# Kernel optimization log

Hardware: AMD Instinct MI355X
Metric: run time of the kernel (lower is better)

The kernel has to match this reference:

```python
import jax, jax.numpy as jnp
import numpy as np

B, T, C = 1, 2048, 1024
H = 16
HD = C // H
BLOCK = 2048
NEG = float('-inf')

def setup_inputs() -> dict:
    key = jax.random.key(0)
    ks = jax.random.split(key, 6)
    x = jax.random.normal(ks[0], (B, T, C), dtype=jnp.float32)
    cumulative_scores = jax.random.normal(ks[1], (B, T), dtype=jnp.float32) * 0.1
    padding_mask = jnp.ones((B, T), dtype=jnp.float32)
    token_index = jax.random.randint(ks[2], (B, T), 0, BLOCK).astype(jnp.int64)
    w_attn = jax.random.normal(ks[3], (C, 3 * C), dtype=jnp.float32) * (1.0 / np.sqrt(C))
    b_attn = jnp.zeros((3 * C,), dtype=jnp.float32)
    w_proj = jax.random.normal(ks[4], (C, C), dtype=jnp.float32) * (1.0 / np.sqrt(C))
    b_proj = jnp.zeros((C,), dtype=jnp.float32)
    return dict(x=x, cumulative_scores=cumulative_scores, padding_mask=padding_mask,
                token_index=token_index, w_attn=w_attn, b_attn=b_attn,
                w_proj=w_proj, b_proj=b_proj)

def _rotate_half(z):
    z1, z2 = z[..., : z.shape[-1] // 2], z[..., z.shape[-1] // 2 :]
    return jnp.concatenate((-z2, z1), axis=-1)

def reference(x, cumulative_scores, padding_mask, token_index, w_attn, b_attn, w_proj, b_proj):
    # fused QKV projection
    qkv = x @ w_attn + b_attn                      # (B,T,3C)
    q, k, v = jnp.split(qkv, 3, axis=2)
    q = q.reshape(B, T, H, HD).transpose(0, 2, 1, 3)  # (B,H,T,HD)
    k = k.reshape(B, T, H, HD).transpose(0, 2, 1, 3)
    v = v.reshape(B, T, H, HD).transpose(0, 2, 1, 3)

    # dynamic per-token RoPE positions: global token counts (original scatter
    # broadcasts indices over batch, so counts are global across all batches)
    cnt = jnp.zeros((BLOCK,), jnp.float32).at[token_index.reshape(-1)].add(1.0)
    per_tok = (1.0 / (cnt + 1e-10))[token_index]       # (B,T)
    partial = jnp.cumsum(per_tok, axis=-1)             # (B,T) fractional positions

    inv_freq = 1.0 / (10000.0 ** (jnp.arange(0, HD, 2, dtype=jnp.float32) / HD))
    freqs = partial[..., None] * inv_freq              # (B,T,HD/2)
    emb = jnp.concatenate((freqs, freqs), axis=-1)     # (B,T,HD)
    cos = jnp.cos(emb)[:, None]                        # (B,1,T,HD)
    sin = jnp.sin(emb)[:, None]
    q = q * cos + _rotate_half(q) * sin
    k = k * cos + _rotate_half(k) * sin

    # 'fork' plan: overwrite last channel
    q = q.at[..., -1].set(1.0)
    k = k.at[..., -1].set(jnp.broadcast_to(cumulative_scores[:, None, :], (B, H, T)))

    # additive causal + padding mask (B,T,T)
    causal = jnp.where(jnp.tril(jnp.ones((T, T), jnp.bool_)), 0.0, NEG)
    pm = jnp.take_along_axis(padding_mask, token_index, axis=1)     # (B,T)
    outer = pm[:, :, None] * pm[:, None, :]
    pad_add = jnp.where(outer.astype(jnp.bool_), 0.0, NEG)
    mask = causal[None, :, :] + pad_add                              # (B,T,T)

    # scale v by exp(cumulative_scores)
    v = v * jnp.exp(cumulative_scores)[:, None, :, None]

    scores = jnp.einsum('bhqd,bhkd->bhqk', q, k) / np.sqrt(HD) + mask[:, None]
    probs = jax.nn.softmax(scores, axis=-1)
    y = jnp.einsum('bhqk,bhkd->bhqd', probs, v)        # (B,H,T,HD)
    y = y.transpose(0, 2, 1, 3).reshape(B, T, C)
    return y @ w_proj + b_proj
```

## Files before the change

### kernel.cpp

```cpp
#include <hip/hip_runtime.h>
#include <math.h>

#define T 2048
#define C 1024
#define H 16
#define HD 64
#define N3 (3*C)
#define NBLOCK 2048

typedef __attribute__((ext_vector_type(8))) short bf16x8;
typedef __attribute__((ext_vector_type(4))) float f32x4;

#define MFMA16(a, b, c) __builtin_amdgcn_mfma_f32_16x16x32_bf16((a), (b), (c), 0, 0, 0)

__device__ inline short f2bf(float f) {
    unsigned u; __builtin_memcpy(&u, &f, 4);
    unsigned r = (u + 0x7fffu + ((u >> 16) & 1u)) >> 16;
    return (short)r;
}
__device__ inline float bf2f(short s) {
    unsigned u = ((unsigned)(unsigned short)s) << 16;
    float f; __builtin_memcpy(&f, &u, 4);
    return f;
}

__device__ inline void gload_lds16(const void* g, void* l) {
    __builtin_amdgcn_global_load_lds((const __attribute__((address_space(1))) unsigned int*)g,
                                     (__attribute__((address_space(3))) unsigned int*)l,
                                     16, 0, 0);
}

__global__ __launch_bounds__(256) void pre_kernel(const float* __restrict__ x,
                                                  const float* __restrict__ w_attn,
                                                  const float* __restrict__ w_proj,
                                                  const int* __restrict__ tok,
                                                  const float* __restrict__ padmask,
                                                  short* __restrict__ xb,
                                                  short* __restrict__ wabT,
                                                  short* __restrict__ wpbT,
                                                  float* __restrict__ partial,
                                                  float* __restrict__ pm_tok) {
    int bid = blockIdx.x;
    int tid = threadIdx.x;
    if (bid == 3072) {
        __shared__ float cntS[NBLOCK];
        __shared__ float sums[256];
        #pragma unroll
        for (int j = 0; j < 8; ++j) cntS[tid * 8 + j] = 0.0f;
        __syncthreads();
        int tk[8];
        #pragma unroll
        for (int j = 0; j < 8; ++j) {
            tk[j] = tok[tid * 8 + j];
            atomicAdd(&cntS[tk[j]], 1.0f);
        }
        __syncthreads();
        float vals[8];
        float s = 0.0f;
        #pragma unroll
        for (int j = 0; j < 8; ++j) {
            s += 1.0f / (cntS[tk[j]] + 1e-10f);
            vals[j] = s;
            pm_tok[tid * 8 + j] = padmask[tk[j]];
        }
        sums[tid] = s;
        __syncthreads();
        for (int off = 1; off < 256; off <<= 1) {
            float v = (tid >= off) ? sums[tid - off] : 0.0f;
            __syncthreads();
            sums[tid] += v;
            __syncthreads();
        }
        float offset = (tid > 0) ? sums[tid - 1] : 0.0f;
        #pragma unroll
        for (int j = 0; j < 8; ++j) partial[tid * 8 + j] = offset + vals[j];
        return;
    }
    if (bid < 2048) {
        int i = bid * 1024 + tid * 4;
        float4 v = *(const float4*)(x + i);
        short4 o;
        o.x = f2bf(v.x); o.y = f2bf(v.y); o.z = f2bf(v.z); o.w = f2bf(v.w);
        *(short4*)(xb + i) = o;
        return;
    }
    __shared__ float S[64][65];
    const float* in; short* out; int Kd, Nd, bx, by;
    if (bid < 2816) {
        int b = bid - 2048;
        bx = b % 48; by = b / 48;
        in = w_attn; out = wabT; Kd = C; Nd = N3;
    } else {
        int b = bid - 2816;
        bx = b % 16; by = b / 16;
        in = w_proj; out = wpbT; Kd = C; Nd = C;
    }
    int n0 = bx * 64, k0 = by * 64;
    #pragma unroll
    for (int i = 0; i < 16; ++i) {
        int lin = tid + i * 256;
        int r = lin >> 6, c = lin & 63;
        S[r][c] = in[(size_t)(k0 + r) * Nd + n0 + c];
    }
    __syncthreads();
    #pragma unroll
    for (int i = 0; i < 16; ++i) {
        int lin = tid + i * 256;
        int rn = lin >> 6, ck = lin & 63;
        out[(size_t)(n0 + rn) * Kd + k0 + ck] = f2bf(S[ck][rn]);
    }
}

template <int OUT_BF16>
__global__ __launch_bounds__(256) void gemm_bt64(const short* __restrict__ A,
                                                 const short* __restrict__ Bt,
                                                 const float* __restrict__ bias,
                                                 void* __restrict__ Cout,
                                                 int M, int N, int K) {
    __shared__ alignas(16) short As[64 * 32];
    __shared__ alignas(16) short Bs[128 * 32];
    int tid = threadIdx.x;
    int m0 = blockIdx.y * 64, n0 = blockIdx.x * 128;
    int w = tid >> 6, l = tid & 63;
    int wm = (w >> 1) * 32, wn = (w & 1) * 64;
    int lq = l & 15, g = l >> 4;
    int prow = l >> 2, pcol = (l & 3) * 8;
    f32x4 acc[2][4] = {};
    for (int k0 = 0; k0 < K; k0 += 32) {
        {
            int rowA = w * 16 + prow;
            gload_lds16(A + (size_t)(m0 + rowA) * K + k0 + pcol, As + w * 512);
            #pragma unroll
            for (int i = 0; i < 2; ++i) {
                int c = w * 2 + i;
                int row = c * 16 + prow;
                gload_lds16(Bt + (size_t)(n0 + row) * K + k0 + pcol, Bs + c * 512);
            }
        }
        __syncthreads();
        bf16x8 af[2], bfr[4];
        #pragma unroll
        for (int f = 0; f < 2; ++f)
            af[f] = *(const bf16x8*)(As + (wm + f * 16 + lq) * 32 + g * 8);
        #pragma unroll
        for (int j = 0; j < 4; ++j)
            bfr[j] = *(const bf16x8*)(Bs + (wn + j * 16 + lq) * 32 + g * 8);
        #pragma unroll
        for (int fi = 0; fi < 2; ++fi)
            #pragma unroll
            for (int fj = 0; fj < 4; ++fj)
                acc[fi][fj] = MFMA16(af[fi], bfr[fj], acc[fi][fj]);
        __syncthreads();
    }
    #pragma unroll
    for (int fi = 0; fi < 2; ++fi)
        #pragma unroll
        for (int fj = 0; fj < 4; ++fj)
            #pragma unroll
            for (int r = 0; r < 4; ++r) {
                int m = m0 + wm + fi * 16 + g * 4 + r;
                int n = n0 + wn + fj * 16 + lq;
                float v = acc[fi][fj][r] + bias[n];
                if (OUT_BF16) ((short*)Cout)[(size_t)m * N + n] = f2bf(v);
                else          ((float*)Cout)[(size_t)m * N + n] = v;
            }
}

__global__ __launch_bounds__(256) void ropevt(short* __restrict__ qkvb,
                                              const float* __restrict__ partial,
                                              const float* __restrict__ cumsc,
                                              const float* __restrict__ pm_tok,
                                              short* __restrict__ vbT) {
    __shared__ alignas(16) short S[64][72];
    __shared__ float efs[64];
    int bid = blockIdx.x;
    int tid = threadIdx.x;
    if (bid < 512) {
        int tg = tid >> 6, l = tid & 63;
        int t = bid * 4 + tg;
        int j = l & 31;
        float inv = exp2f(-(float)j * (13.287712379549449f / 32.0f));
        float ang = partial[t] * inv;
        float cs_own = cosf(ang), sn_own = sinf(ang);
        float csc = cumsc[t];
        float pmv = pm_tok[t];
        float qfix = (pmv != 0.0f) ? 1.0f : 0.0f;
        float kfix = (pmv != 0.0f) ? csc : -1e20f;

        int h = l >> 2, jb = (l & 3) * 8;
        short* row = qkvb + (size_t)t * N3;
        int c1 = h * 64 + jb;
        bf16x8 qlo = *(const bf16x8*)(row + c1);
        bf16x8 qhi = *(const bf16x8*)(row + c1 + 32);
        bf16x8 klo = *(const bf16x8*)(row + C + c1);
        bf16x8 khi = *(const bf16x8*)(row + C + c1 + 32);
        bf16x8 qlo2, qhi2, klo2, khi2;
        #pragma unroll
        for (int i = 0; i < 8; ++i) {
            float cs = __shfl(cs_own, jb + i);
            float sn = __shfl(sn_own, jb + i);
            float q1 = bf2f(qlo[i]), q2 = bf2f(qhi[i]);
            float k1 = bf2f(klo[i]), k2 = bf2f(khi[i]);
            float q2n = q2 * cs + q1 * sn;
            float k2n = k2 * cs + k1 * sn;
            if (jb + i == 31) { q2n = qfix; k2n = kfix; }
            qlo2[i] = f2bf(q1 * cs - q2 * sn);
            qhi2[i] = f2bf(q2n);
            klo2[i] = f2bf(k1 * cs - k2 * sn);
            khi2[i] = f2bf(k2n);
        }
        *(bf16x8*)(row + c1) = qlo2;
        *(bf16x8*)(row + c1 + 32) = qhi2;
        *(bf16x8*)(row + C + c1) = klo2;
        *(bf16x8*)(row + C + c1 + 32) = khi2;
        return;
    }
    int b = bid - 512;
    int h = b >> 5;
    int t0 = (b & 31) * 64;
    if (tid < 64) efs[tid] = __expf(cumsc[t0 + tid]);
    __syncthreads();
    #pragma unroll
    for (int e = 0; e < 2; ++e) {
        int s = tid * 2 + e;
        int r = s >> 3, c8 = (s & 7) * 8;
        bf16x8 v = *(const bf16x8*)(qkvb + (size_t)(t0 + r) * N3 + 2 * C + h * 64 + c8);
        float ef = efs[r];
        bf16x8 o;
        #pragma unroll
        for (int i = 0; i < 8; ++i) o[i] = f2bf(bf2f(v[i]) * ef);
        *(bf16x8*)&S[r][c8] = o;
    }
    __syncthreads();
    #pragma unroll
    for (int e = 0; e < 2; ++e) {
        int s = tid * 2 + e;
        int d = s >> 3, t8 = (s & 7) * 8;
        bf16x8 o;
        #pragma unroll
        for (int i = 0; i < 8; ++i) o[i] = S[t8 + i][d];
        *(bf16x8*)(vbT + (size_t)(h * 64 + d) * T + t0 + t8) = o;
    }
}

__global__ __launch_bounds__(256) void attn_flash(const short* __restrict__ qkvb,
                                                  const short* __restrict__ vbT,
                                                  short* __restrict__ yb) {
    __shared__ alignas(16) short Kt[2][64 * 64];
    __shared__ alignas(16) short Vt[2][64 * 64];
    __shared__ alignas(16) short Ps[4][16][72];

    int b = blockIdx.x;
    int h, qt;
    if (b < 256) { h = b & 15; qt = 31 - (b >> 4); }
    else         { int c2 = b - 256; h = c2 & 15; qt = c2 >> 4; }
    int tid = threadIdx.x;
    int w = tid >> 6, l = tid & 63;
    int lq = l & 15, g = l >> 4;
    int qrl = w * 16 + lq;

    const short* qbase = qkvb + (size_t)(qt * 64 + qrl) * N3 + h * 64;
    bf16x8 qf0 = *(const bf16x8*)(qbase + g * 8);
    bf16x8 qf1 = *(const bf16x8*)(qbase + 32 + g * 8);

    f32x4 accO[4] = {};
    float lsum = 0.0f;

    int srow = tid >> 3, scol = (tid & 7) * 8;
    const short* kgb = qkvb + C + h * 64 + scol;
    const short* vgb = vbT + (size_t)(h * 64) * T + scol;
    int wb0 = srow * 128 + ((scol * 2) ^ ((srow & 7) << 4));
    int wb1 = (srow + 32) * 128 + ((scol * 2) ^ ((srow & 7) << 4));

    auto do_tile = [&](int cur, bool masked) {
        const char* Kc = (const char*)Kt[cur];
        const char* Vc = (const char*)Vt[cur];
        f32x4 s[4] = {};
        __builtin_amdgcn_s_setprio(1);
        #pragma unroll
        for (int f = 0; f < 4; ++f) {
            int row = f * 16 + lq;
            const char* kr_ = Kc + row * 128;
            int sw = (row & 7) << 4;
            bf16x8 a0 = *(const bf16x8*)(kr_ + ((g * 16) ^ sw));
            bf16x8 a1 = *(const bf16x8*)(kr_ + ((64 + g * 16) ^ sw));
            s[f] = MFMA16(a0, qf0, s[f]);
            s[f] = MFMA16(a1, qf1, s[f]);
        }
        __builtin_amdgcn_s_setprio(0);
        float p[16];
        #pragma unroll
        for (int f = 0; f < 4; ++f)
            #pragma unroll
            for (int r = 0; r < 4; ++r) {
                float sv = s[f][r] * 0.125f;
                if (masked) {
                    int kl = f * 16 + g * 4 + r;
                    sv = (kl > qrl) ? -INFINITY : sv;
                }
                float pv = __expf(sv);
                p[f * 4 + r] = pv;
                lsum += pv;
            }
        #pragma unroll
        for (int f = 0; f < 4; ++f) {
            unsigned u0, u1;
            asm("v_cvt_pk_bf16_f32 %0, %1, %2" : "=v"(u0) : "v"(p[f * 4 + 0]), "v"(p[f * 4 + 1]));
            asm("v_cvt_pk_bf16_f32 %0, %1, %2" : "=v"(u1) : "v"(p[f * 4 + 2]), "v"(p[f * 4 + 3]));
            uint2 uu; uu.x = u0; uu.y = u1;
            *(uint2*)&Ps[w][lq][f * 16 + g * 4] = uu;
        }
        __builtin_amdgcn_s_setprio(1);
        #pragma unroll
        for (int kh = 0; kh < 2; ++kh) {
            bf16x8 pa = *(const bf16x8*)&Ps[w][lq][kh * 32 + g * 8];
            #pragma unroll
            for (int f = 0; f < 4; ++f) {
                int vrow = f * 16 + lq;
                const char* vr_ = Vc + vrow * 128;
                bf16x8 vb = *(const bf16x8*)(vr_ + (((kh * 32 + g * 8) * 2) ^ ((vrow & 7) << 4)));
                accO[f] = MFMA16(pa, vb, accO[f]);
            }
        }
        __builtin_amdgcn_s_setprio(0);
    };

    uint4 kr0 = *(const uint4*)(kgb + (size_t)srow * N3);
    uint4 kr1 = *(const uint4*)(kgb + (size_t)(srow + 32) * N3);
    uint4 vr0 = *(const uint4*)(vgb + (size_t)srow * T);
    uint4 vr1 = *(const uint4*)(vgb + (size_t)(srow + 32) * T);
    *(uint4*)((char*)Kt[0] + wb0) = kr0;
    *(uint4*)((char*)Kt[0] + wb1) = kr1;
    *(uint4*)((char*)Vt[0] + wb0) = vr0;
    *(uint4*)((char*)Vt[0] + wb1) = vr1;
    __syncthreads();

    for (int t = 0; t < qt; ++t) {
        int kn = (t + 1) * 64;
        kr0 = *(const uint4*)(kgb + (size_t)(kn + srow) * N3);
        kr1 = *(const uint4*)(kgb + (size_t)(kn + srow + 32) * N3);
        vr0 = *(const uint4*)(vgb + (size_t)srow * T + kn);
        vr1 = *(const uint4*)(vgb + (size_t)(srow + 32) * T + kn);

        do_tile(t & 1, false);

        int nxt = (t & 1) ^ 1;
        *(uint4*)((char*)Kt[nxt] + wb0) = kr0;
        *(uint4*)((char*)Kt[nxt] + wb1) = kr1;
        *(uint4*)((char*)Vt[nxt] + wb0) = vr0;
        *(uint4*)((char*)Vt[nxt] + wb1) = vr1;
        __syncthreads();
    }
    do_tile(qt & 1, true);

    lsum += __shfl_xor(lsum, 16);
    lsum += __shfl_xor(lsum, 32);
    float linv_own = 1.0f / lsum;
    float li[4];
    #pragma unroll
    for (int r = 0; r < 4; ++r) li[r] = __shfl(linv_own, g * 4 + r);

    #pragma unroll
    for (int f = 0; f < 4; ++f)
        #pragma unroll
        for (int r = 0; r < 4; ++r) {
            int trow = qt * 64 + w * 16 + g * 4 + r;
            yb[(size_t)trow * C + h * 64 + f * 16 + lq] = f2bf(accO[f][r] * li[r]);
        }
}

extern "C" void kernel_launch(void* const* d_in, const int* in_sizes, int n_in,
                              void* d_out, int out_size, void* d_ws, size_t ws_size,
                              hipStream_t stream) {
    const float* x       = (const float*)d_in[0];
    const float* cumsc   = (const float*)d_in[1];
    const float* padmask = (const float*)d_in[2];
    const int*   tok     = (const int*)d_in[3];
    const float* w_attn  = (const float*)d_in[4];
    const float* b_attn  = (const float*)d_in[5];
    const float* w_proj  = (const float*)d_in[6];
    const float* b_proj  = (const float*)d_in[7];
    float* out = (float*)d_out;

    float* part   = (float*)d_ws;
    float* pm_tok = part + 2048;
    short* xb     = (short*)(pm_tok + 2048);
    short* wabT   = xb + (size_t)T * C;
    short* wpbT   = wabT + (size_t)N3 * C;
    short* qkvb   = wpbT + (size_t)C * C;
    short* vbT    = qkvb + (size_t)T * N3;
    short* yb     = vbT + (size_t)C * T;

    pre_kernel<<<3073, 256, 0, stream>>>(x, w_attn, w_proj, tok, padmask,
                                         xb, wabT, wpbT, part, pm_tok);
    gemm_bt64<1><<<dim3(N3 / 128, T / 64), 256, 0, stream>>>(xb, wabT, b_attn, qkvb, T, N3, C);
    ropevt<<<1024, 256, 0, stream>>>(qkvb, part, cumsc, pm_tok, vbT);
    attn_flash<<<512, 256, 0, stream>>>(qkvb, vbT, yb);
    gemm_bt64<0><<<dim3(C / 128, T / 64), 256, 0, stream>>>(yb, wpbT, b_proj, out, T, C, C);
}
```

Before: 92.20 us.

## Fuse RoPE, fork fix-up and V scale/transpose into QKV GEMM epilogue

Removes the separate ropevt kernel by applying RoPE, the last-channel overwrite, and the exp(cumulative_scores) scaling with transposed V store directly in the QKV GEMM epilogue. This saves one kernel launch plus a full read and rewrite of the Q/K/V buffer. In exchange the epilogue does more work, including per-element sincos and strided transposed short4 stores for V. V is also no longer written to qkvb, and the fast __sincosf may be less accurate than cosf/sinf.

```diff
diff --git a/kernel.cpp b/kernel.cpp
--- a/kernel.cpp
+++ b/kernel.cpp
@@ -111,12 +111,16 @@
     }
 }
 
-template <int OUT_BF16>
+template <int OUT_BF16, int EPI>
 __global__ __launch_bounds__(256) void gemm_bt64(const short* __restrict__ A,
                                                  const short* __restrict__ Bt,
                                                  const float* __restrict__ bias,
                                                  void* __restrict__ Cout,
-                                                 int M, int N, int K) {
+                                                 int M, int N, int K,
+                                                 const float* __restrict__ partial,
+                                                 const float* __restrict__ cumsc,
+                                                 const float* __restrict__ pm_tok,
+                                                 short* __restrict__ vbT) {
     __shared__ alignas(16) short As[64 * 32];
     __shared__ alignas(16) short Bs[128 * 32];
     int tid = threadIdx.x;
@@ -152,94 +156,79 @@
                 acc[fi][fj] = MFMA16(af[fi], bfr[fj], acc[fi][fj]);
         __syncthreads();
     }
-    #pragma unroll
-    for (int fi = 0; fi < 2; ++fi)
-        #pragma unroll
-        for (int fj = 0; fj < 4; ++fj)
-            #pragma unroll
-            for (int r = 0; r < 4; ++r) {
-                int m = m0 + wm + fi * 16 + g * 4 + r;
-                int n = n0 + wn + fj * 16 + lq;
-                float v = acc[fi][fj][r] + bias[n];
-                if (OUT_BF16) ((short*)Cout)[(size_t)m * N + n] = f2bf(v);
-                else          ((float*)Cout)[(size_t)m * N + n] = v;
+
+    if (EPI == 0) {
+        #pragma unroll
+        for (int fi = 0; fi < 2; ++fi)
+            #pragma unroll
+            for (int fj = 0; fj < 4; ++fj)
+                #pragma unroll
+                for (int r = 0; r < 4; ++r) {
+                    int m = m0 + wm + fi * 16 + g * 4 + r;
+                    int n = n0 + wn + fj * 16 + lq;
+                    float v = acc[fi][fj][r] + bias[n];
+                    if (OUT_BF16) ((short*)Cout)[(size_t)m * N + n] = f2bf(v);
+                    else          ((float*)Cout)[(size_t)m * N + n] = v;
+                }
+    } else {
+        short* Cb = (short*)Cout;
+        int cb = n0 + wn;
+        int section = cb >> 10;
+        float b0 = bias[cb + lq],      b1 = bias[cb + 16 + lq];
+        float b2 = bias[cb + 32 + lq], b3 = bias[cb + 48 + lq];
+        if (section < 2) {
+            bool isQ = (section == 0);
+            float inv0 = exp2f(-(float)lq * (13.287712379549449f / 32.0f));
+            float inv1 = exp2f(-(float)(lq + 16) * (13.287712379549449f / 32.0f));
+            #pragma unroll
+            for (int fi = 0; fi < 2; ++fi)
+                #pragma unroll
+                for (int r = 0; r < 4; ++r) {
+                    int trow = m0 + wm + fi * 16 + g * 4 + r;
+                    float pt = partial[trow];
+                    float sn0, cs0, sn1, cs1;
+                    __sincosf(pt * inv0, &sn0, &cs0);
+                    __sincosf(pt * inv1, &sn1, &cs1);
+                    float a0 = acc[fi][0][r] + b0;
+                    float a1 = acc[fi][1][r] + b1;
+                    float a2 = acc[fi][2][r] + b2;
+                    float a3 = acc[fi][3][r] + b3;
+                    float lo0 = a0 * cs0 - a2 * sn0;
+                    float hi0 = a2 * cs0 + a0 * sn0;
+                    float lo1 = a1 * cs1 - a3 * sn1;
+                    float hi1 = a3 * cs1 + a1 * sn1;
+                    if (lq == 15) {
+                        float pm = pm_tok[trow];
+                        hi1 = isQ ? ((pm != 0.0f) ? 1.0f : 0.0f)
+                                  : ((pm != 0.0f) ? cumsc[trow] : -1e20f);
+                    }
+                    size_t base = (size_t)trow * N3 + cb;
+                    Cb[base + lq]      = f2bf(lo0);
+                    Cb[base + 16 + lq] = f2bf(lo1);
+                    Cb[base + 32 + lq] = f2bf(hi0);
+                    Cb[base + 48 + lq] = f2bf(hi1);
+                }
+        } else {
+            int h = (cb - 2 * C) >> 6;
+            #pragma unroll
+            for (int fi = 0; fi < 2; ++fi) {
+                int tb = m0 + wm + fi * 16 + g * 4;
+                float ef[4];
+                #pragma unroll
+                for (int r = 0; r < 4; ++r) ef[r] = __expf(cumsc[tb + r]);
+                #pragma unroll
+                for (int fj = 0; fj < 4; ++fj) {
+                    int d = fj * 16 + lq;
+                    float bv = (fj == 0) ? b0 : (fj == 1) ? b1 : (fj == 2) ? b2 : b3;
+                    short4 o;
+                    o.x = f2bf((acc[fi][fj][0] + bv) * ef[0]);
+                    o.y = f2bf((acc[fi][fj][1] + bv) * ef[1]);
+                    o.z = f2bf((acc[fi][fj][2] + bv) * ef[2]);
+                    o.w = f2bf((acc[fi][fj][3] + bv) * ef[3]);
+                    *(short4*)(vbT + (size_t)(h * 64 + d) * T + tb) = o;
+                }
             }
-}
-
-__global__ __launch_bounds__(256) void ropevt(short* __restrict__ qkvb,
-                                              const float* __restrict__ partial,
-                                              const float* __restrict__ cumsc,
-                                              const float* __restrict__ pm_tok,
-                                              short* __restrict__ vbT) {
-    __shared__ alignas(16) short S[64][72];
-    __shared__ float efs[64];
-    int bid = blockIdx.x;
-    int tid = threadIdx.x;
-    if (bid < 512) {
-        int tg = tid >> 6, l = tid & 63;
-        int t = bid * 4 + tg;
-        int j = l & 31;
-        float inv = exp2f(-(float)j * (13.287712379549449f / 32.0f));
-        float ang = partial[t] * inv;
-        float cs_own = cosf(ang), sn_own = sinf(ang);
-        float csc = cumsc[t];
-        float pmv = pm_tok[t];
-        float qfix = (pmv != 0.0f) ? 1.0f : 0.0f;
-        float kfix = (pmv != 0.0f) ? csc : -1e20f;
-
-        int h = l >> 2, jb = (l & 3) * 8;
-        short* row = qkvb + (size_t)t * N3;
-        int c1 = h * 64 + jb;
-        bf16x8 qlo = *(const bf16x8*)(row + c1);
-        bf16x8 qhi = *(const bf16x8*)(row + c1 + 32);
-        bf16x8 klo = *(const bf16x8*)(row + C + c1);
-        bf16x8 khi = *(const bf16x8*)(row + C + c1 + 32);
-        bf16x8 qlo2, qhi2, klo2, khi2;
-        #pragma unroll
-        for (int i = 0; i < 8; ++i) {
-            float cs = __shfl(cs_own, jb + i);
-            float sn = __shfl(sn_own, jb + i);
-            float q1 = bf2f(qlo[i]), q2 = bf2f(qhi[i]);
-            float k1 = bf2f(klo[i]), k2 = bf2f(khi[i]);
-            float q2n = q2 * cs + q1 * sn;
-            float k2n = k2 * cs + k1 * sn;
-            if (jb + i == 31) { q2n = qfix; k2n = kfix; }
-            qlo2[i] = f2bf(q1 * cs - q2 * sn);
-            qhi2[i] = f2bf(q2n);
-            klo2[i] = f2bf(k1 * cs - k2 * sn);
-            khi2[i] = f2bf(k2n);
-        }
-        *(bf16x8*)(row + c1) = qlo2;
-        *(bf16x8*)(row + c1 + 32) = qhi2;
-        *(bf16x8*)(row + C + c1) = klo2;
-        *(bf16x8*)(row + C + c1 + 32) = khi2;
-        return;
-    }
-    int b = bid - 512;
-    int h = b >> 5;
-    int t0 = (b & 31) * 64;
-    if (tid < 64) efs[tid] = __expf(cumsc[t0 + tid]);
-    __syncthreads();
-    #pragma unroll
-    for (int e = 0; e < 2; ++e) {
-        int s = tid * 2 + e;
-        int r = s >> 3, c8 = (s & 7) * 8;
-        bf16x8 v = *(const bf16x8*)(qkvb + (size_t)(t0 + r) * N3 + 2 * C + h * 64 + c8);
-        float ef = efs[r];
-        bf16x8 o;
-        #pragma unroll
-        for (int i = 0; i < 8; ++i) o[i] = f2bf(bf2f(v[i]) * ef);
-        *(bf16x8*)&S[r][c8] = o;
-    }
-    __syncthreads();
-    #pragma unroll
-    for (int e = 0; e < 2; ++e) {
-        int s = tid * 2 + e;
-        int d = s >> 3, t8 = (s & 7) * 8;
-        bf16x8 o;
-        #pragma unroll
-        for (int i = 0; i < 8; ++i) o[i] = S[t8 + i][d];
-        *(bf16x8*)(vbT + (size_t)(h * 64 + d) * T + t0 + t8) = o;
+        }
     }
 }
 
@@ -393,8 +382,9 @@
 
     pre_kernel<<<3073, 256, 0, stream>>>(x, w_attn, w_proj, tok, padmask,
                                          xb, wabT, wpbT, part, pm_tok);
-    gemm_bt64<1><<<dim3(N3 / 128, T / 64), 256, 0, stream>>>(xb, wabT, b_attn, qkvb, T, N3, C);
-    ropevt<<<1024, 256, 0, stream>>>(qkvb, part, cumsc, pm_tok, vbT);
+    gemm_bt64<1, 1><<<dim3(N3 / 128, T / 64), 256, 0, stream>>>(
+        xb, wabT, b_attn, qkvb, T, N3, C, part, cumsc, pm_tok, vbT);
     attn_flash<<<512, 256, 0, stream>>>(qkvb, vbT, yb);
-    gemm_bt64<0><<<dim3(C / 128, T / 64), 256, 0, stream>>>(yb, wpbT, b_proj, out, T, C, C);
-}
+    gemm_bt64<0, 0><<<dim3(C / 128, T / 64), 256, 0, stream>>>(
+        yb, wpbT, b_proj, out, T, C, C, nullptr, nullptr, nullptr, nullptr);
+}
```

Result: faster. 88.53 us (-4.0%).
